# Performance work log

Hardware: AMD Instinct MI355X
Metric: run time of the kernel (lower is better)

Reference implementation:

```python
import jax, jax.numpy as jnp
import numpy as np

M, N, E, IN, C, HID, TOPK = 4, 50000, 400000, 128, 128, 256, 2
NEG_SLOPE = 0.2


def setup_inputs() -> dict:
    key = jax.random.key(0)
    k = jax.random.split(key, 16)
    s = lambda f: 1.0 / np.sqrt(f)
    return {
        "x_src": jax.random.normal(k[0], (M, N, IN), jnp.float32),
        "x_dst": jax.random.normal(k[1], (N, IN), jnp.float32),
        "src_idx": jax.random.randint(k[2], (M, E), 0, N),
        "dst_idx": jax.random.randint(k[3], (M, E), 0, N),
        "proj_Ws": jax.random.normal(k[4], (M, IN, C), jnp.float32) * s(IN),
        "proj_bs": jnp.zeros((M, C), jnp.float32),
        "projd_W": jax.random.normal(k[5], (IN, C), jnp.float32) * s(IN),
        "projd_b": jnp.zeros((C,), jnp.float32),
        "lin_src": jax.random.normal(k[6], (M, C), jnp.float32) * s(C),
        "lin_dst": jax.random.normal(k[7], (M, C), jnp.float32) * s(C),
        "gm_W1": jax.random.normal(k[8], (C, C), jnp.float32) * s(C),
        "gm_b1": jnp.zeros((C,), jnp.float32),
        "gm_W2": jax.random.normal(k[9], (C, C), jnp.float32) * s(C),
        "gm_b2": jnp.zeros((C,), jnp.float32),
        "gate_W1": jax.random.normal(k[10], (M * C, HID), jnp.float32) * s(M * C),
        "gate_b1": jnp.zeros((HID,), jnp.float32),
        "gate_W2": jax.random.normal(k[11], (HID, M), jnp.float32) * s(HID),
        "gate_b2": jnp.zeros((M,), jnp.float32),
        "exp_W1": jax.random.normal(k[12], (M, C, HID), jnp.float32) * s(C),
        "exp_b1": jnp.zeros((M, HID), jnp.float32),
        "exp_W2": jax.random.normal(k[13], (M, HID, C), jnp.float32) * s(HID),
        "exp_b2": jnp.zeros((M, C), jnp.float32),
    }


def _propagate(xs_t, asrc_t, adst_t, si, di, recept_t):
    # GAT-style attention message passing for one edge type.
    # xs_t: [N,C] projected src feats, asrc_t/adst_t: [N] attn logits,
    # si/di: [E] edge endpoints, recept_t: [N] per-dst-node receptivity gate.
    e = jax.nn.leaky_relu(asrc_t[si] + adst_t[di], NEG_SLOPE)  # [E]
    emax = jax.ops.segment_max(e, di, num_segments=N)
    ez = jnp.exp(e - emax[di])
    den = jax.ops.segment_sum(ez, di, num_segments=N)
    alpha = ez / (den[di] + 1e-16)                             # softmax per dst node
    msg = xs_t[si] * (alpha * recept_t[di])[:, None]           # [E,C]
    return jax.ops.segment_sum(msg, di, num_segments=N)       # [N,C]


def reference(x_src, x_dst, src_idx, dst_idx, proj_Ws, proj_bs, projd_W, projd_b,
              lin_src, lin_dst, gm_W1, gm_b1, gm_W2, gm_b2,
              gate_W1, gate_b1, gate_W2, gate_b2,
              exp_W1, exp_b1, exp_W2, exp_b2):
    # --- SynapticConvLayer (eval path, heads=1) ---
    xs = jnp.einsum('mni,mic->mnc', x_src, proj_Ws) + proj_bs[:, None, :]  # [M,N,C]
    xd = x_dst @ projd_W + projd_b                                          # [N,C]
    a_src = jnp.einsum('mnc,mc->mn', xs, lin_src)
    a_dst = jnp.einsum('nc,mc->mn', xd[None].repeat(M, 0) * 0 + xd[None], lin_dst) if False else jnp.einsum('nc,mc->mn', xd, lin_dst)
    prop = jax.vmap(_propagate)
    out1 = prop(xs, a_src, a_dst, src_idx, dst_idx, jnp.ones((M, N), xs.dtype))
    # receptivity from grad_map surrogate (inference branch)
    feat_diff = out1 - xd[None]                                            # [M,N,C]
    mo = jax.nn.sigmoid(jax.nn.relu(feat_diff @ gm_W1 + gm_b1) @ gm_W2 + gm_b2)
    gd = (mo * feat_diff).mean(axis=-1)                                    # [M,N]
    recept = gd / (jnp.abs(gd) + 1e-8)                                     # L2-norm over the singleton head dim == abs
    out2 = prop(xs, a_src, a_dst, src_idx, dst_idx, recept)
    feats = jax.nn.relu(out2)                                              # [M,N,C] per-edge-type dst features
    # --- SourceExpertMoE ---
    feats_nm = feats.transpose(1, 0, 2)                                    # [N,M,C]
    gate_in = feats_nm.reshape(N, M * C)
    logits = jax.nn.relu(gate_in @ gate_W1 + gate_b1) @ gate_W2 + gate_b2
    gw = jax.nn.softmax(logits, axis=1)
    scores = gw + recept.T                                                 # gate weights + receptivity
    top_w, top_i = jax.lax.top_k(scores, TOPK)
    top_w = top_w / top_w.sum(axis=1, keepdims=True)
    # expert e applied to source-e features for every node (dense, then gather top-k)
    h = jax.nn.relu(jnp.einsum('nmi,mih->nmh', feats_nm, exp_W1) + exp_b1)
    out_all = jnp.einsum('nmh,mho->nmo', h, exp_W2) + exp_b2               # [N,M,C]
    sel = jnp.take_along_axis(out_all, top_i[:, :, None], axis=1)          # [N,K,C]
    final = (sel * top_w[:, :, None]).sum(axis=1)                          # [N,C]
    return final
```

## Files before the change

### kernel.cpp

```cpp
#include <hip/hip_runtime.h>
#include <hip/hip_bf16.h>
#include <math.h>

#define M_  4
#define N_  50000
#define E_  400000
#define IN_ 128
#define C_  128
#define HID_ 256

template<int AMODE, int EPI, int ASCALE>
__global__ void __launch_bounds__(256) gemm11(
    const float* A, const float* A2, const float* __restrict__ B,
    const float* __restrict__ bias, float* Cmat,
    const int* __restrict__ idx, const int* __restrict__ cnts,
    const float* __restrict__ AS, const float* __restrict__ fdbuf,
    const int* __restrict__ roff,
    int R, int K, int NC,
    long long aBatch, long long bBatch, int biasBatch, long long cBatch,
    long long strideM)
{
  __shared__ float As[8][64];
  __shared__ float Bs[8][128];
  __shared__ float red[(EPI == 5) ? 64 * 17 : 1];

  const int tid = threadIdx.x;
  const int b = blockIdx.y;
  const int Reff = (AMODE == 4 || AMODE == 5) ? cnts[b] : (cnts ? cnts[0] : R);
  const int rb = blockIdx.x * 64;
  if (rb >= Reff) return;
  const int cb = blockIdx.z * 128;

  const float* Ab = (AMODE == 2) ? A : (A + (long long)b * aBatch);
  const float* Bb = B + (long long)b * bBatch + cb;
  const float* biasb = bias + (long long)b * biasBatch + cb;

  const int ar = tid >> 1;
  const int ak = (tid & 1) * 4;
  const int r_a = rb + ar;
  const bool a_ok = (tid < 128) && (r_a < Reff);
  long long a_row = 0;
  float a_rs = 0.f;
  if (a_ok) {
    if (AMODE == 4) {
      int orow = idx[(long long)b * N_ + r_a];
      a_row = (long long)orow * K;
      if (ASCALE == 2) a_rs = AS[(long long)b * N_ + orow];
    } else if (AMODE == 5) {
      a_row = (long long)(roff[b] + r_a) * K;
    } else if (AMODE == 2) {
      a_row = (long long)r_a * 128;
    } else {
      a_row = (long long)r_a * K;
    }
  }
  const int bk = tid >> 5;
  const int bc = (tid & 31) * 4;

  const int tx = tid & 15;
  const int ty = tid >> 4;

  float acc[4][8];
  #pragma unroll
  for (int i = 0; i < 4; ++i)
    #pragma unroll
    for (int j = 0; j < 8; ++j) acc[i][j] = 0.f;

  const int nt = K >> 3;
  float4 av = make_float4(0.f, 0.f, 0.f, 0.f), bv;

#define LOAD_TILE(k0)                                                          \
  {                                                                            \
    if (a_ok) {                                                                \
      if (AMODE == 2) {                                                        \
        int kk0 = (k0) + ak;                                                   \
        av = *(const float4*)(Ab + (long long)(kk0 >> 7) * strideM + a_row +   \
                              (kk0 & 127));                                    \
        if (ASCALE == 1) {                                                     \
          float rs = AS[(kk0 >> 7) * N_ + r_a];                                \
          av.x = fmaxf(av.x * rs, 0.f); av.y = fmaxf(av.y * rs, 0.f);          \
          av.z = fmaxf(av.z * rs, 0.f); av.w = fmaxf(av.w * rs, 0.f);          \
        }                                                                      \
      } else {                                                                 \
        av = *(const float4*)(Ab + a_row + (k0) + ak);                         \
        if (AMODE == 4 && ASCALE == 2) {                                       \
          av.x = fmaxf(av.x * a_rs, 0.f); av.y = fmaxf(av.y * a_rs, 0.f);      \
          av.z = fmaxf(av.z * a_rs, 0.f); av.w = fmaxf(av.w * a_rs, 0.f);      \
        }                                                                      \
      }                                                                        \
    } else {                                                                   \
      av = make_float4(0.f, 0.f, 0.f, 0.f);                                    \
    }                                                                          \
    bv = *(const float4*)(Bb + (long long)((k0) + bk) * NC + bc);              \
  }

  LOAD_TILE(0)

  for (int t = 0; t < nt; ++t) {
    __syncthreads();
    if (tid < 128) {
      As[ak + 0][ar] = av.x; As[ak + 1][ar] = av.y;
      As[ak + 2][ar] = av.z; As[ak + 3][ar] = av.w;
    }
    *(float4*)(&Bs[bk][bc]) = bv;
    __syncthreads();

    if (t + 1 < nt) LOAD_TILE((t + 1) * 8)

    #pragma unroll
    for (int kk = 0; kk < 8; ++kk) {
      float4 a4 = *(float4*)(&As[kk][ty * 4]);
      float4 blo = *(float4*)(&Bs[kk][tx * 4]);
      float4 bhi = *(float4*)(&Bs[kk][64 + tx * 4]);
      float a_[4] = {a4.x, a4.y, a4.z, a4.w};
      float b8[8] = {blo.x, blo.y, blo.z, blo.w, bhi.x, bhi.y, bhi.z, bhi.w};
      #pragma unroll
      for (int i = 0; i < 4; ++i)
        #pragma unroll
        for (int j = 0; j < 8; ++j)
          acc[i][j] += a_[i] * b8[j];
    }
  }
#undef LOAD_TILE

  if (EPI == 5) {
    #pragma unroll
    for (int i = 0; i < 4; ++i) {
      const int r_local = ty * 4 + i;
      const int r = rb + r_local;
      if (r < Reff) {
        const float* fdrow = fdbuf + (long long)b * cBatch + (long long)r * 128;
        const float* xdrow = A2 + (long long)r * 128;
        float4 flo = *(const float4*)(fdrow + tx * 4);
        float4 fhi = *(const float4*)(fdrow + 64 + tx * 4);
        float4 xlo = *(const float4*)(xdrow + tx * 4);
        float4 xhi = *(const float4*)(xdrow + 64 + tx * 4);
        float fd8[8] = {flo.x - xlo.x, flo.y - xlo.y, flo.z - xlo.z, flo.w - xlo.w,
                        fhi.x - xhi.x, fhi.y - xhi.y, fhi.z - xhi.z, fhi.w - xhi.w};
        float p = 0.f;
        #pragma unroll
        for (int j = 0; j < 8; ++j) {
          const int c = (j < 4 ? tx * 4 + j : 64 + tx * 4 + (j - 4));
          float mo = 1.f / (1.f + expf(-(acc[i][j] + biasb[c])));
          p += mo * fd8[j];
        }
        red[r_local * 17 + tx] = p;
      }
    }
    __syncthreads();
    if (tid < 64) {
      const int r = rb + tid;
      if (r < Reff) {
        float s = 0.f;
        #pragma unroll
        for (int t = 0; t < 16; ++t) s += red[tid * 17 + t];
        float gd = s / 128.f;
        Cmat[(long long)b * N_ + r] = gd / (fabsf(gd) + 1e-8f);
      }
    }
    return;
  }

  #pragma unroll
  for (int i = 0; i < 4; ++i) {
    const int r = rb + ty * 4 + i;
    if (r >= Reff) continue;
    long long crow;
    if (EPI == 7) crow = (long long)(roff[b] + r) * NC + cb;
    else if (EPI == 9) crow = (long long)(roff[b] + r) * 128 + cb;
    else crow = (long long)b * cBatch + (long long)r * NC + cb;
    const float* subrow = (EPI == 6) ? (fdbuf + (long long)r * 128 + cb) : nullptr;
    #pragma unroll
    for (int j = 0; j < 8; ++j) {
      const int c = (j < 4 ? tx * 4 + j : 64 + tx * 4 + (j - 4));
      float v = acc[i][j] + biasb[c];
      if (EPI == 6) v = fmaxf(v - subrow[c], 0.f);
      if (EPI == 1 || EPI == 7) v = fmaxf(v, 0.f);
      Cmat[crow + c] = v;
    }
  }
}

__global__ void attn_logit_kernel(const float* __restrict__ X, const float* __restrict__ lin,
                                  float* __restrict__ out, int Nn, int perM)
{
  int m = blockIdx.y;
  int w = blockIdx.x * (blockDim.x >> 6) + (threadIdx.x >> 6);
  int lane = threadIdx.x & 63;
  if (w >= Nn) return;
  long long row = perM ? ((long long)m * Nn + w) : (long long)w;
  const float* xr = X + row * 128;
  const float* lr = lin + m * 128;
  float acc = xr[lane] * lr[lane] + xr[lane + 64] * lr[lane + 64];
  #pragma unroll
  for (int off = 32; off > 0; off >>= 1) acc += __shfl_down(acc, off);
  if (lane == 0) out[(long long)m * Nn + w] = acc;
}

__global__ void count_kernel(const int* __restrict__ dst, int* __restrict__ cnt, int Nn)
{
  int e = blockIdx.x * blockDim.x + threadIdx.x;
  int m = blockIdx.y;
  if (e >= E_) return;
  atomicAdd(&cnt[(long long)m * Nn + dst[(long long)m * E_ + e]], 1);
}

__global__ void chunkscan_kernel(const int* __restrict__ cnt, int* __restrict__ rowptr,
                                 int* __restrict__ chunktot)
{
  int m = blockIdx.y, ch = blockIdx.x;
  int base = ch * 1024;
  const int* c = cnt + (long long)m * N_;
  int* rp = rowptr + (long long)m * (N_ + 1);
  __shared__ int sums[256];
  int t = threadIdx.x;
  int v[4]; int s = 0;
  #pragma unroll
  for (int k = 0; k < 4; ++k) {
    int i = base + t * 4 + k;
    v[k] = (i < N_) ? c[i] : 0;
    s += v[k];
  }
  sums[t] = s;
  __syncthreads();
  for (int off = 1; off < 256; off <<= 1) {
    int x = (t >= off) ? sums[t - off] : 0;
    __syncthreads();
    sums[t] += x;
    __syncthreads();
  }
  int run = sums[t] - s;
  #pragma unroll
  for (int k = 0; k < 4; ++k) {
    int i = base + t * 4 + k;
    run += v[k];
    if (i < N_) rp[i + 1] = run;
  }
  if (t == 255) chunktot[m * 64 + ch] = sums[255];
}

__global__ void scantot_kernel(int* __restrict__ chunktot, int nch)
{
  int m = threadIdx.x;
  if (m >= M_) return;
  int run = 0;
  for (int ch = 0; ch < nch; ++ch) {
    int v = chunktot[m * 64 + ch];
    chunktot[m * 64 + ch] = run;
    run += v;
  }
}

__global__ void addoff_kernel(int* __restrict__ rowptr, const int* __restrict__ chunktot)
{
  int m = blockIdx.y, ch = blockIdx.x;
  int off = chunktot[m * 64 + ch];
  int t = threadIdx.x;
  int* rp = rowptr + (long long)m * (N_ + 1);
  #pragma unroll
  for (int k = 0; k < 4; ++k) {
    int i = ch * 1024 + t * 4 + k;
    if (i < N_) rp[i + 1] += off;
  }
  if (ch == 0 && t == 0) rp[0] = 0;
}

__global__ void scatter_kernel(const int* __restrict__ dst, const int* __restrict__ rowptr,
                               int* __restrict__ fill, int* __restrict__ col, int Nn)
{
  int e = blockIdx.x * blockDim.x + threadIdx.x;
  int m = blockIdx.y;
  if (e >= E_) return;
  int d = dst[(long long)m * E_ + e];
  int pos = rowptr[(long long)m * (Nn + 1) + d] + atomicAdd(&fill[(long long)m * Nn + d], 1);
  col[(long long)m * E_ + pos] = e;
}

__global__ void sortbucket_kernel(const int* __restrict__ rowptr, int* __restrict__ col, int Nn)
{
  int n = blockIdx.x * blockDim.x + threadIdx.x;
  int m = blockIdx.y;
  if (n >= Nn) return;
  const int* rp = rowptr + (long long)m * (Nn + 1);
  int* c = col + (long long)m * E_;
  int b = rp[n], e = rp[n + 1];
  for (int i = b + 1; i < e; ++i) {
    int v = c[i]; int j = i - 1;
    while (j >= b && c[j] > v) { c[j + 1] = c[j]; --j; }
    c[j + 1] = v;
  }
}

__global__ void edge_e_kernel(const int* __restrict__ src, const int* __restrict__ dst,
                              const float* __restrict__ asrc, const float* __restrict__ adst,
                              float* __restrict__ e_edge)
{
  int e = blockIdx.x * blockDim.x + threadIdx.x;
  int m = blockIdx.y;
  if (e >= E_) return;
  long long off = (long long)m * E_ + e;
  float v = asrc[(long long)m * N_ + src[off]] + adst[(long long)m * N_ + dst[off]];
  e_edge[off] = (v >= 0.f) ? v : 0.2f * v;
}

__global__ void alpha_kernel(const int* __restrict__ rowptr, const int* __restrict__ col,
                             const int* __restrict__ src, const float* __restrict__ e_edge,
                             float* __restrict__ alpha, int* __restrict__ src_csr)
{
  int n = blockIdx.x * blockDim.x + threadIdx.x;
  int m = blockIdx.y;
  if (n >= N_) return;
  const int* rp = rowptr + (long long)m * (N_ + 1);
  const int* cl = col + (long long)m * E_;
  const int* sr = src + (long long)m * E_;
  const float* ee = e_edge + (long long)m * E_;
  float* al = alpha + (long long)m * E_;
  int* sc = src_csr + (long long)m * E_;
  int b = rp[n], en = rp[n + 1];
  if (b == en) return;
  float emax = -INFINITY;
  for (int j = b; j < en; ++j) emax = fmaxf(emax, ee[cl[j]]);
  float den = 0.f;
  for (int j = b; j < en; ++j) {
    int eid = cl[j];
    float ez = expf(ee[eid] - emax);
    den += ez;
    al[j] = ez;
    sc[j] = sr[eid];
  }
  float inv = 1.f / (den + 1e-16f);
  for (int j = b; j < en; ++j) al[j] *= inv;
}

__global__ void prop2_kernel(const float* __restrict__ xs, const int* __restrict__ rowptr,
                             const float* __restrict__ alpha, const int* __restrict__ src_csr,
                             float* __restrict__ out)
{
  int d = blockIdx.x * 2 + (threadIdx.x >> 7);
  int m = blockIdx.y;
  int c = threadIdx.x & 127;
  if (d >= N_) return;
  const int* rp = rowptr + (long long)m * (N_ + 1);
  const float* al = alpha + (long long)m * E_;
  const int* sc = src_csr + (long long)m * E_;
  const float* xsm = xs + (long long)m * N_ * 128;
  int b = rp[d], en = rp[d + 1];
  float acc = 0.f;
  int j = b;
  for (; j + 3 < en; j += 4) {
    float a0 = al[j], a1 = al[j + 1], a2 = al[j + 2], a3 = al[j + 3];
    int s0 = sc[j], s1 = sc[j + 1], s2 = sc[j + 2], s3 = sc[j + 3];
    float x0 = xsm[(long long)s0 * 128 + c];
    float x1 = xsm[(long long)s1 * 128 + c];
    float x2 = xsm[(long long)s2 * 128 + c];
    float x3 = xsm[(long long)s3 * 128 + c];
    acc += a0 * x0; acc += a1 * x1; acc += a2 * x2; acc += a3 * x3;
  }
  for (; j < en; ++j)
    acc += al[j] * xsm[(long long)sc[j] * 128 + c];
  out[((long long)m * N_ + d) * 128 + c] = acc;
}

__global__ void gate_logits_kernel(const float* __restrict__ h, const float* __restrict__ W2,
                                   const float* __restrict__ b2, float* __restrict__ logits, int Nn)
{
  int w = blockIdx.x * (blockDim.x >> 6) + (threadIdx.x >> 6);
  int lane = threadIdx.x & 63;
  if (w >= Nn) return;
  const float* hr = h + (long long)w * 256;
  float a0 = 0.f, a1 = 0.f, a2 = 0.f, a3 = 0.f;
  for (int j = lane; j < 256; j += 64) {
    float hv = hr[j];
    a0 += hv * W2[j * 4 + 0];
    a1 += hv * W2[j * 4 + 1];
    a2 += hv * W2[j * 4 + 2];
    a3 += hv * W2[j * 4 + 3];
  }
  #pragma unroll
  for (int off = 32; off > 0; off >>= 1) {
    a0 += __shfl_down(a0, off);
    a1 += __shfl_down(a1, off);
    a2 += __shfl_down(a2, off);
    a3 += __shfl_down(a3, off);
  }
  if (lane == 0) {
    long long o = (long long)w * 4;
    logits[o + 0] = a0 + b2[0];
    logits[o + 1] = a1 + b2[1];
    logits[o + 2] = a2 + b2[2];
    logits[o + 3] = a3 + b2[3];
  }
}

__global__ void topk_kernel(const float* __restrict__ logits, const float* __restrict__ recept,
                            float* __restrict__ wsel, int Nn)
{
  int n = blockIdx.x * blockDim.x + threadIdx.x;
  if (n >= Nn) return;
  float l[4];
  #pragma unroll
  for (int m = 0; m < 4; ++m) l[m] = logits[(long long)n * 4 + m];
  float mx = fmaxf(fmaxf(l[0], l[1]), fmaxf(l[2], l[3]));
  float e[4], s = 0.f;
  #pragma unroll
  for (int m = 0; m < 4; ++m) { e[m] = expf(l[m] - mx); s += e[m]; }
  float sc[4];
  #pragma unroll
  for (int m = 0; m < 4; ++m) sc[m] = e[m] / s + recept[(long long)m * Nn + n];
  int i0 = 0; float v0 = sc[0];
  #pragma unroll
  for (int m = 1; m < 4; ++m) if (sc[m] > v0) { v0 = sc[m]; i0 = m; }
  int i1 = -1; float v1 = -INFINITY;
  #pragma unroll
  for (int m = 0; m < 4; ++m) { if (m == i0) continue; if (sc[m] > v1) { v1 = sc[m]; i1 = m; } }
  float ts = v0 + v1;
  float w0 = v0 / ts, w1 = v1 / ts;
  #pragma unroll
  for (int m = 0; m < 4; ++m)
    wsel[(long long)m * Nn + n] = (m == i0) ? w0 : ((m == i1) ? w1 : 0.f);
}

__global__ void compact_kernel(const float* __restrict__ wsel, int* __restrict__ idx,
                               int* __restrict__ posmn, int* __restrict__ cnts, int Nn)
{
  int n = blockIdx.x * blockDim.x + threadIdx.x;
  if (n >= Nn) return;
  #pragma unroll
  for (int m = 0; m < 4; ++m) {
    if (wsel[(long long)m * Nn + n] != 0.f) {
      int p = atomicAdd(&cnts[m], 1);
      idx[(long long)m * Nn + p] = n;
      posmn[(long long)m * Nn + n] = p;
    }
  }
}

__global__ void prefix4_kernel(const int* __restrict__ cnts, int* __restrict__ off)
{
  if (threadIdx.x == 0) {
    int r = 0;
    #pragma unroll
    for (int m = 0; m < 4; ++m) { off[m] = r; r += cnts[m]; }
  }
}

__global__ void combine_kernel(const float* __restrict__ outp, const float* __restrict__ wsel,
                               const int* __restrict__ posmn, const int* __restrict__ expoff,
                               float* __restrict__ fin)
{
  long long i = (long long)blockIdx.x * blockDim.x + threadIdx.x;
  if (i >= (long long)N_ * 32) return;
  int n = (int)(i >> 5);
  int c4 = (int)(i & 31) * 4;
  float4 acc = make_float4(0.f, 0.f, 0.f, 0.f);
  #pragma unroll
  for (int m = 0; m < 4; ++m) {
    float w = wsel[(long long)m * N_ + n];
    if (w != 0.f) {
      int p = expoff[m] + posmn[(long long)m * N_ + n];
      float4 v = *(const float4*)(outp + (long long)p * 128 + c4);
      acc.x += w * v.x; acc.y += w * v.y; acc.z += w * v.z; acc.w += w * v.w;
    }
  }
  *(float4*)(fin + (long long)n * 128 + c4) = acc;
}

extern "C" void kernel_launch(void* const* d_in, const int* in_sizes, int n_in,
                              void* d_out, int out_size, void* d_ws, size_t ws_size,
                              hipStream_t stream) {
  const float* x_src   = (const float*)d_in[0];
  const float* x_dst   = (const float*)d_in[1];
  const int*   src_idx = (const int*)d_in[2];
  const int*   dst_idx = (const int*)d_in[3];
  const float* proj_Ws = (const float*)d_in[4];
  const float* proj_bs = (const float*)d_in[5];
  const float* projd_W = (const float*)d_in[6];
  const float* projd_b = (const float*)d_in[7];
  const float* lin_src = (const float*)d_in[8];
  const float* lin_dst = (const float*)d_in[9];
  const float* gm_W1   = (const float*)d_in[10];
  const float* gm_b1   = (const float*)d_in[11];
  const float* gm_W2   = (const float*)d_in[12];
  const float* gm_b2   = (const float*)d_in[13];
  const float* gate_W1 = (const float*)d_in[14];
  const float* gate_b1 = (const float*)d_in[15];
  const float* gate_W2 = (const float*)d_in[16];
  const float* gate_b2 = (const float*)d_in[17];
  const float* exp_W1  = (const float*)d_in[18];
  const float* exp_b1  = (const float*)d_in[19];
  const float* exp_W2  = (const float*)d_in[20];
  const float* exp_b2  = (const float*)d_in[21];
  float* final_out = (float*)d_out;

  float* ws = (float*)d_ws;
  float* bufA   = ws;
  float* bufB   = ws + 25600000LL;
  float* xd     = ws + 51200000LL;
  float* asrc   = ws + 57600000LL;
  float* adst   = ws + 57800000LL;
  float* recept = ws + 58000000LL;
  float* wsel   = ws + 58200000LL;
  float* logits = ws + 58400000LL;
  float* e_edge = ws + 58600000LL;
  float* alpha  = ws + 60200000LL;
  float* xdW1   = ws + 61800000LL;
  float* zbuf   = ws + 68200000LL;
  int*   ibase  = (int*)(ws + 68300000LL);
  int*   rowptr = ibase;
  int*   col    = ibase + 200004;
  int*   cnt    = ibase + 1800004;
  int*   expidx = cnt;
  int*   expcnt = ibase + 2000004;
  int*   src_csr= ibase + 2000008;
  int*   chunktot = ibase + 3600008;
  int*   expoff = ibase + 3600264;
  int*   posmn  = ibase + 3600268;

  const long long NC = (long long)N_ * C_;
  const int RB = (N_ + 63) / 64;
  const int NCH = (N_ + 1023) / 1024;

  hipMemsetAsync(cnt, 0, (size_t)M_ * N_ * sizeof(int), stream);
  hipMemsetAsync(zbuf, 0, 128 * sizeof(float), stream);
  count_kernel<<<dim3((E_ + 255) / 256, M_), 256, 0, stream>>>(dst_idx, cnt, N_);
  chunkscan_kernel<<<dim3(NCH, M_), 256, 0, stream>>>(cnt, rowptr, chunktot);
  scantot_kernel<<<1, 64, 0, stream>>>(chunktot, NCH);
  addoff_kernel<<<dim3(NCH, M_), 256, 0, stream>>>(rowptr, chunktot);
  hipMemsetAsync(cnt, 0, (size_t)M_ * N_ * sizeof(int), stream);
  scatter_kernel<<<dim3((E_ + 255) / 256, M_), 256, 0, stream>>>(dst_idx, rowptr, cnt, col, N_);
  sortbucket_kernel<<<dim3((N_ + 255) / 256, M_), 256, 0, stream>>>(rowptr, col, N_);

  gemm11<0, 0, 0><<<dim3(RB, 1, 1), 256, 0, stream>>>(
      x_dst, nullptr, projd_W, projd_b, xd, nullptr, nullptr, nullptr, nullptr,
      nullptr, N_, IN_, C_, 0, 0, 0, 0, 0);
  attn_logit_kernel<<<dim3((N_ + 3) / 4, M_), 256, 0, stream>>>(xd, lin_dst, adst, N_, 0);

  gemm11<0, 0, 0><<<dim3(RB, 1, 1), 256, 0, stream>>>(
      xd, nullptr, gm_W1, zbuf, xdW1, nullptr, nullptr, nullptr, nullptr,
      nullptr, N_, C_, C_, 0, 0, 0, 0, 0);

  gemm11<0, 0, 0><<<dim3(RB, M_, 1), 256, 0, stream>>>(
      x_src, nullptr, proj_Ws, proj_bs, bufA, nullptr, nullptr, nullptr, nullptr,
      nullptr, N_, IN_, C_, NC, (long long)IN_ * C_, C_, NC, 0);
  attn_logit_kernel<<<dim3((N_ + 3) / 4, M_), 256, 0, stream>>>(bufA, lin_src, asrc, N_, 1);

  edge_e_kernel<<<dim3((E_ + 255) / 256, M_), 256, 0, stream>>>(
      src_idx, dst_idx, asrc, adst, e_edge);
  alpha_kernel<<<dim3((N_ + 255) / 256, M_), 256, 0, stream>>>(
      rowptr, col, src_idx, e_edge, alpha, src_csr);

  prop2_kernel<<<dim3((N_ + 1) / 2, M_), 256, 0, stream>>>(bufA, rowptr, alpha, src_csr, bufB);

  gemm11<0, 6, 0><<<dim3(RB, M_, 1), 256, 0, stream>>>(
      bufB, nullptr, gm_W1, gm_b1, bufA, nullptr, nullptr, nullptr, xdW1,
      nullptr, N_, C_, C_, NC, 0, 0, NC, 0);
  gemm11<0, 5, 0><<<dim3(RB, M_, 1), 256, 0, stream>>>(
      bufA, xd, gm_W2, gm_b2, recept, nullptr, nullptr, nullptr, bufB,
      nullptr, N_, C_, C_, NC, 0, 0, NC, 0);

  gemm11<2, 1, 1><<<dim3(RB, 1, 2), 256, 0, stream>>>(
      bufB, nullptr, gate_W1, gate_b1, bufA, nullptr, nullptr, recept, nullptr,
      nullptr, N_, M_ * C_, HID_, 0, 0, 0, 0, NC);
  gate_logits_kernel<<<dim3((N_ + 3) / 4), 256, 0, stream>>>(bufA, gate_W2, gate_b2, logits, N_);
  topk_kernel<<<(N_ + 255) / 256, 256, 0, stream>>>(logits, recept, wsel, N_);

  hipMemsetAsync(expcnt, 0, 4 * sizeof(int), stream);
  compact_kernel<<<(N_ + 255) / 256, 256, 0, stream>>>(wsel, expidx, posmn, expcnt, N_);
  prefix4_kernel<<<1, 64, 0, stream>>>(expcnt, expoff);

  gemm11<4, 7, 2><<<dim3(RB, M_, 2), 256, 0, stream>>>(
      bufB, nullptr, exp_W1, exp_b1, bufA, expidx, expcnt, recept, nullptr,
      expoff, N_, C_, HID_, NC, (long long)C_ * HID_, HID_, 0, 0);
  gemm11<5, 9, 0><<<dim3(RB, M_, 1), 256, 0, stream>>>(
      bufA, nullptr, exp_W2, exp_b2, bufB, expidx, expcnt, nullptr, nullptr,
      expoff, N_, HID_, C_, 0, (long long)HID_ * C_, C_, 0, 0);
  combine_kernel<<<(int)(((long long)N_ * 32 + 255) / 256), 256, 0, stream>>>(
      bufB, wsel, posmn, expoff, final_out);
}
```

Measured before the change: 1.272 ms.

## Double GEMM K-tile to 16 and fuse src attention logit into projection GEMM

The shared GEMM now loads 16-deep K tiles per iteration, so all 256 threads load A instead of half, and there are half as many barrier pairs. The source-projection GEMM gains an epilogue that dots each output row with lin_src and reduces through shared memory to write asrc directly. This removes the separate attn_logit pass that re-read the full projected source features. Shared-memory use doubles and per-thread register pressure rises slightly, which may affect occupancy.

```diff
diff --git a/kernel.cpp b/kernel.cpp
--- a/kernel.cpp
+++ b/kernel.cpp
@@ -10,19 +10,19 @@
 #define HID_ 256
 
 template<int AMODE, int EPI, int ASCALE>
-__global__ void __launch_bounds__(256) gemm11(
+__global__ void __launch_bounds__(256) gemm14(
     const float* A, const float* A2, const float* __restrict__ B,
     const float* __restrict__ bias, float* Cmat,
     const int* __restrict__ idx, const int* __restrict__ cnts,
     const float* __restrict__ AS, const float* __restrict__ fdbuf,
-    const int* __restrict__ roff,
+    const int* __restrict__ roff, float* aux,
     int R, int K, int NC,
     long long aBatch, long long bBatch, int biasBatch, long long cBatch,
     long long strideM)
 {
-  __shared__ float As[8][64];
-  __shared__ float Bs[8][128];
-  __shared__ float red[(EPI == 5) ? 64 * 17 : 1];
+  __shared__ float As[16][64];
+  __shared__ float Bs[16][128];
+  __shared__ float red[(EPI == 5 || EPI == 10) ? 64 * 17 : 1];
 
   const int tid = threadIdx.x;
   const int b = blockIdx.y;
@@ -35,10 +35,10 @@
   const float* Bb = B + (long long)b * bBatch + cb;
   const float* biasb = bias + (long long)b * biasBatch + cb;
 
-  const int ar = tid >> 1;
-  const int ak = (tid & 1) * 4;
+  const int ar = tid >> 2;
+  const int ak = (tid & 3) * 4;
   const int r_a = rb + ar;
-  const bool a_ok = (tid < 128) && (r_a < Reff);
+  const bool a_ok = (r_a < Reff);
   long long a_row = 0;
   float a_rs = 0.f;
   if (a_ok) {
@@ -59,6 +59,7 @@
 
   const int tx = tid & 15;
   const int ty = tid >> 4;
+  const int fr = ty * 4;
 
   float acc[4][8];
   #pragma unroll
@@ -66,8 +67,8 @@
     #pragma unroll
     for (int j = 0; j < 8; ++j) acc[i][j] = 0.f;
 
-  const int nt = K >> 3;
-  float4 av = make_float4(0.f, 0.f, 0.f, 0.f), bv;
+  const int nt = K >> 4;
+  float4 av = make_float4(0.f, 0.f, 0.f, 0.f), bv0, bv1;
 
 #define LOAD_TILE(k0)                                                          \
   {                                                                            \
@@ -91,25 +92,25 @@
     } else {                                                                   \
       av = make_float4(0.f, 0.f, 0.f, 0.f);                                    \
     }                                                                          \
-    bv = *(const float4*)(Bb + (long long)((k0) + bk) * NC + bc);              \
+    bv0 = *(const float4*)(Bb + (long long)((k0) + bk) * NC + bc);             \
+    bv1 = *(const float4*)(Bb + (long long)((k0) + bk + 8) * NC + bc);         \
   }
 
   LOAD_TILE(0)
 
   for (int t = 0; t < nt; ++t) {
     __syncthreads();
-    if (tid < 128) {
-      As[ak + 0][ar] = av.x; As[ak + 1][ar] = av.y;
-      As[ak + 2][ar] = av.z; As[ak + 3][ar] = av.w;
-    }
-    *(float4*)(&Bs[bk][bc]) = bv;
+    As[ak + 0][ar] = av.x; As[ak + 1][ar] = av.y;
+    As[ak + 2][ar] = av.z; As[ak + 3][ar] = av.w;
+    *(float4*)(&Bs[bk][bc]) = bv0;
+    *(float4*)(&Bs[bk + 8][bc]) = bv1;
     __syncthreads();
 
-    if (t + 1 < nt) LOAD_TILE((t + 1) * 8)
+    if (t + 1 < nt) LOAD_TILE((t + 1) * 16)
 
     #pragma unroll
-    for (int kk = 0; kk < 8; ++kk) {
-      float4 a4 = *(float4*)(&As[kk][ty * 4]);
+    for (int kk = 0; kk < 16; ++kk) {
+      float4 a4 = *(float4*)(&As[kk][fr]);
       float4 blo = *(float4*)(&Bs[kk][tx * 4]);
       float4 bhi = *(float4*)(&Bs[kk][64 + tx * 4]);
       float a_[4] = {a4.x, a4.y, a4.z, a4.w};
@@ -126,7 +127,7 @@
   if (EPI == 5) {
     #pragma unroll
     for (int i = 0; i < 4; ++i) {
-      const int r_local = ty * 4 + i;
+      const int r_local = fr + i;
       const int r = rb + r_local;
       if (r < Reff) {
         const float* fdrow = fdbuf + (long long)b * cBatch + (long long)r * 128;
@@ -163,13 +164,14 @@
 
   #pragma unroll
   for (int i = 0; i < 4; ++i) {
-    const int r = rb + ty * 4 + i;
+    const int r = rb + fr + i;
     if (r >= Reff) continue;
     long long crow;
     if (EPI == 7) crow = (long long)(roff[b] + r) * NC + cb;
     else if (EPI == 9) crow = (long long)(roff[b] + r) * 128 + cb;
     else crow = (long long)b * cBatch + (long long)r * NC + cb;
     const float* subrow = (EPI == 6) ? (fdbuf + (long long)r * 128 + cb) : nullptr;
+    float p = 0.f;
     #pragma unroll
     for (int j = 0; j < 8; ++j) {
       const int c = (j < 4 ? tx * 4 + j : 64 + tx * 4 + (j - 4));
@@ -177,19 +179,32 @@
       if (EPI == 6) v = fmaxf(v - subrow[c], 0.f);
       if (EPI == 1 || EPI == 7) v = fmaxf(v, 0.f);
       Cmat[crow + c] = v;
+      if (EPI == 10) p += v * AS[(long long)b * 128 + c];
+    }
+    if (EPI == 10) red[(fr + i) * 17 + tx] = p;
+  }
+  if (EPI == 10) {
+    __syncthreads();
+    if (tid < 64) {
+      const int r = rb + tid;
+      if (r < Reff) {
+        float s = 0.f;
+        #pragma unroll
+        for (int t = 0; t < 16; ++t) s += red[tid * 17 + t];
+        aux[(long long)b * N_ + r] = s;
+      }
     }
   }
 }
 
 __global__ void attn_logit_kernel(const float* __restrict__ X, const float* __restrict__ lin,
-                                  float* __restrict__ out, int Nn, int perM)
+                                  float* __restrict__ out, int Nn)
 {
   int m = blockIdx.y;
   int w = blockIdx.x * (blockDim.x >> 6) + (threadIdx.x >> 6);
   int lane = threadIdx.x & 63;
   if (w >= Nn) return;
-  long long row = perM ? ((long long)m * Nn + w) : (long long)w;
-  const float* xr = X + row * 128;
+  const float* xr = X + (long long)w * 128;
   const float* lr = lin + m * 128;
   float acc = xr[lane] * lr[lane] + xr[lane + 64] * lr[lane + 64];
   #pragma unroll
@@ -530,19 +545,18 @@
   scatter_kernel<<<dim3((E_ + 255) / 256, M_), 256, 0, stream>>>(dst_idx, rowptr, cnt, col, N_);
   sortbucket_kernel<<<dim3((N_ + 255) / 256, M_), 256, 0, stream>>>(rowptr, col, N_);
 
-  gemm11<0, 0, 0><<<dim3(RB, 1, 1), 256, 0, stream>>>(
+  gemm14<0, 0, 0><<<dim3(RB, 1, 1), 256, 0, stream>>>(
       x_dst, nullptr, projd_W, projd_b, xd, nullptr, nullptr, nullptr, nullptr,
-      nullptr, N_, IN_, C_, 0, 0, 0, 0, 0);
-  attn_logit_kernel<<<dim3((N_ + 3) / 4, M_), 256, 0, stream>>>(xd, lin_dst, adst, N_, 0);
-
-  gemm11<0, 0, 0><<<dim3(RB, 1, 1), 256, 0, stream>>>(
+      nullptr, nullptr, N_, IN_, C_, 0, 0, 0, 0, 0);
+  attn_logit_kernel<<<dim3((N_ + 3) / 4, M_), 256, 0, stream>>>(xd, lin_dst, adst, N_);
+
+  gemm14<0, 0, 0><<<dim3(RB, 1, 1), 256, 0, stream>>>(
       xd, nullptr, gm_W1, zbuf, xdW1, nullptr, nullptr, nullptr, nullptr,
-      nullptr, N_, C_, C_, 0, 0, 0, 0, 0);
-
-  gemm11<0, 0, 0><<<dim3(RB, M_, 1), 256, 0, stream>>>(
-      x_src, nullptr, proj_Ws, proj_bs, bufA, nullptr, nullptr, nullptr, nullptr,
-      nullptr, N_, IN_, C_, NC, (long long)IN_ * C_, C_, NC, 0);
-  attn_logit_kernel<<<dim3((N_ + 3) / 4, M_), 256, 0, stream>>>(bufA, lin_src, asrc, N_, 1);
+      nullptr, nullptr, N_, C_, C_, 0, 0, 0, 0, 0);
+
+  gemm14<0, 10, 0><<<dim3(RB, M_, 1), 256, 0, stream>>>(
+      x_src, nullptr, proj_Ws, proj_bs, bufA, nullptr, nullptr, lin_src, nullptr,
+      nullptr, asrc, N_, IN_, C_, NC, (long long)IN_ * C_, C_, NC, 0);
 
   edge_e_kernel<<<dim3((E_ + 255) / 256, M_), 256, 0, stream>>>(
       src_idx, dst_idx, asrc, adst, e_edge);
@@ -551,16 +565,16 @@
 
   prop2_kernel<<<dim3((N_ + 1) / 2, M_), 256, 0, stream>>>(bufA, rowptr, alpha, src_csr, bufB);
 
-  gemm11<0, 6, 0><<<dim3(RB, M_, 1), 256, 0, stream>>>(
+  gemm14<0, 6, 0><<<dim3(RB, M_, 1), 256, 0, stream>>>(
       bufB, nullptr, gm_W1, gm_b1, bufA, nullptr, nullptr, nullptr, xdW1,
-      nullptr, N_, C_, C_, NC, 0, 0, NC, 0);
-  gemm11<0, 5, 0><<<dim3(RB, M_, 1), 256, 0, stream>>>(
+      nullptr, nullptr, N_, C_, C_, NC, 0, 0, NC, 0);
+  gemm14<0, 5, 0><<<dim3(RB, M_, 1), 256, 0, stream>>>(
       bufA, xd, gm_W2, gm_b2, recept, nullptr, nullptr, nullptr, bufB,
-      nullptr, N_, C_, C_, NC, 0, 0, NC, 0);
-
-  gemm11<2, 1, 1><<<dim3(RB, 1, 2), 256, 0, stream>>>(
+      nullptr, nullptr, N_, C_, C_, NC, 0, 0, NC, 0);
+
+  gemm14<2, 1, 1><<<dim3(RB, 1, 2), 256, 0, stream>>>(
       bufB, nullptr, gate_W1, gate_b1, bufA, nullptr, nullptr, recept, nullptr,
-      nullptr, N_, M_ * C_, HID_, 0, 0, 0, 0, NC);
+      nullptr, nullptr, N_, M_ * C_, HID_, 0, 0, 0, 0, NC);
   gate_logits_kernel<<<dim3((N_ + 3) / 4), 256, 0, stream>>>(bufA, gate_W2, gate_b2, logits, N_);
   topk_kernel<<<(N_ + 255) / 256, 256, 0, stream>>>(logits, recept, wsel, N_);
 
@@ -568,12 +582,12 @@
   compact_kernel<<<(N_ + 255) / 256, 256, 0, stream>>>(wsel, expidx, posmn, expcnt, N_);
   prefix4_kernel<<<1, 64, 0, stream>>>(expcnt, expoff);
 
-  gemm11<4, 7, 2><<<dim3(RB, M_, 2), 256, 0, stream>>>(
+  gemm14<4, 7, 2><<<dim3(RB, M_, 2), 256, 0, stream>>>(
       bufB, nullptr, exp_W1, exp_b1, bufA, expidx, expcnt, recept, nullptr,
-      expoff, N_, C_, HID_, NC, (long long)C_ * HID_, HID_, 0, 0);
-  gemm11<5, 9, 0><<<dim3(RB, M_, 1), 256, 0, stream>>>(
+      expoff, nullptr, N_, C_, HID_, NC, (long long)C_ * HID_, HID_, 0, 0);
+  gemm14<5, 9, 0><<<dim3(RB, M_, 1), 256, 0, stream>>>(
       bufA, nullptr, exp_W2, exp_b2, bufB, expidx, expcnt, nullptr, nullptr,
-      expoff, N_, HID_, C_, 0, (long long)HID_ * C_, C_, 0, 0);
+      expoff, nullptr, N_, HID_, C_, 0, (long long)HID_ * C_, C_, 0, 0);
   combine_kernel<<<(int)(((long long)N_ * 32 + 255) / 256), 256, 0, stream>>>(
       bufB, wsel, posmn, expoff, final_out);
 }
```

New measurement: 1.263 ms. Within noise of the previous version (-0.7%).
